# Performance work log

Measured on AMD Instinct MI355X. Metric: run time of the kernel, lower is better.

The kernel has to match this reference:

```python
import jax, jax.numpy as jnp
import numpy as np

DIM = 512


def layer_norm(x, w, b, eps=1e-5):
    mu = jnp.mean(x, axis=-1, keepdims=True)
    var = jnp.var(x, axis=-1, keepdims=True)
    return (x - mu) * jax.lax.rsqrt(var + eps) * w + b


def setup_inputs() -> dict:
    key = jax.random.key(0)
    kx, = jax.random.split(key, 1)
    x = jax.random.normal(kx, (8, 2048, DIM), dtype=jnp.float32)
    ln_w = jnp.ones((DIM,), dtype=jnp.float32)
    ln_b = jnp.zeros((DIM,), dtype=jnp.float32)
    q_diag = jnp.ones((DIM,), dtype=jnp.float32)
    k_diag = jnp.ones((DIM,), dtype=jnp.float32)
    v_diag = jnp.ones((DIM,), dtype=jnp.float32)
    return {"x": x, "ln_w": ln_w, "ln_b": ln_b,
            "q_diag": q_diag, "k_diag": k_diag, "v_diag": v_diag}


def reference(x, ln_w, ln_b, q_diag, k_diag, v_diag):
    # x: [B, N, D]
    xn = layer_norm(x, ln_w, ln_b)
    q = xn * q_diag
    k = xn * k_diag
    v = xn * v_diag
    scale = 1.0 / jnp.sqrt(jnp.float32(xn.shape[-1]))
    sim = jnp.einsum('bnd,bmd->bnm', q, k) * scale  # [B, N, N]
    attn = jax.nn.softmax(sim, axis=-1)
    atn_x = jnp.einsum('bnm,bmd->bnd', attn, v)
    # dropout is identity at inference (p=0)
    return xn + atn_x
```

## Files before the change

kernel.cpp:

```cpp
#include <hip/hip_runtime.h>
#include <hip/hip_bf16.h>
#include <stdint.h>
#include <math.h>

typedef __bf16 bf16_t;
typedef bf16_t bf16x8 __attribute__((ext_vector_type(8)));
typedef float f32x4 __attribute__((ext_vector_type(4)));

#define B_DIM 8
#define N_DIM 2048
#define D_DIM 512
#define QK_SCALE_L2E 0.063758716f
#define M_SHIFT2 5.7707801635558536f

#define KOFF 0
#define VOFF 65536
#define SMEM_ATTN 163840

__device__ __forceinline__ bf16_t f2bf(float f) {
    uint32_t u = __builtin_bit_cast(uint32_t, f);
    u += 0x7FFFu + ((u >> 16) & 1u);
    uint16_t h = (uint16_t)(u >> 16);
    return __builtin_bit_cast(bf16_t, h);
}

__device__ __forceinline__ float fexp2(float x) {
    float r;
    asm("v_exp_f32 %0, %1" : "=v"(r) : "v"(x));
    return r;
}

__global__ __launch_bounds__(512) void prep_fused(
    const float* __restrict__ x, const float* __restrict__ w, const float* __restrict__ bia,
    const float* __restrict__ qd, const float* __restrict__ kd, const float* __restrict__ vd,
    bf16_t* __restrict__ xnb, float* __restrict__ xnf,
    bf16_t* __restrict__ qb, bf16_t* __restrict__ kb, bf16_t* __restrict__ vT)
{
    extern __shared__ char pmem[];
    bf16_t (*vt)[512] = (bf16_t(*)[512])pmem;

    const int bid = blockIdx.x;
    const int b  = bid >> 5;
    const int n0 = (bid & 31) * 64;
    const int tid  = threadIdx.x;
    const int wid  = tid >> 6;
    const int lane = tid & 63;
    const int d    = lane * 8;

    float wv[8], bv[8], qv[8], kv[8], vv[8];
    {
        float4 t;
        t = *(const float4*)(w  + d);     wv[0]=t.x; wv[1]=t.y; wv[2]=t.z; wv[3]=t.w;
        t = *(const float4*)(w  + d + 4); wv[4]=t.x; wv[5]=t.y; wv[6]=t.z; wv[7]=t.w;
        t = *(const float4*)(bia+ d);     bv[0]=t.x; bv[1]=t.y; bv[2]=t.z; bv[3]=t.w;
        t = *(const float4*)(bia+ d + 4); bv[4]=t.x; bv[5]=t.y; bv[6]=t.z; bv[7]=t.w;
        t = *(const float4*)(qd + d);     qv[0]=t.x; qv[1]=t.y; qv[2]=t.z; qv[3]=t.w;
        t = *(const float4*)(qd + d + 4); qv[4]=t.x; qv[5]=t.y; qv[6]=t.z; qv[7]=t.w;
        t = *(const float4*)(kd + d);     kv[0]=t.x; kv[1]=t.y; kv[2]=t.z; kv[3]=t.w;
        t = *(const float4*)(kd + d + 4); kv[4]=t.x; kv[5]=t.y; kv[6]=t.z; kv[7]=t.w;
        t = *(const float4*)(vd + d);     vv[0]=t.x; vv[1]=t.y; vv[2]=t.z; vv[3]=t.w;
        t = *(const float4*)(vd + d + 4); vv[4]=t.x; vv[5]=t.y; vv[6]=t.z; vv[7]=t.w;
    }

    for (int r = 0; r < 8; r++) {
        int nl = wid*8 + r;
        size_t row  = (size_t)b*N_DIM + n0 + nl;
        size_t base = row*D_DIM + d;
        float xv[8];
        {
            float4 a0 = *(const float4*)(x + base);
            float4 a1 = *(const float4*)(x + base + 4);
            xv[0]=a0.x; xv[1]=a0.y; xv[2]=a0.z; xv[3]=a0.w;
            xv[4]=a1.x; xv[5]=a1.y; xv[6]=a1.z; xv[7]=a1.w;
        }
        float s = 0.f, s2 = 0.f;
        #pragma unroll
        for (int j = 0; j < 8; j++) { s += xv[j]; s2 += xv[j]*xv[j]; }
        #pragma unroll
        for (int m = 1; m < 64; m <<= 1) {
            s  += __shfl_xor(s,  m);
            s2 += __shfl_xor(s2, m);
        }
        float mu   = s  * (1.f/512.f);
        float var  = s2 * (1.f/512.f) - mu*mu;
        float rstd = rsqrtf(var + 1e-5f);

        float xo[8];
        bf16x8 qo, ko, xb, vb;
        #pragma unroll
        for (int j = 0; j < 8; j++) {
            float v = (xv[j] - mu) * rstd * wv[j] + bv[j];
            xo[j] = v;
            xb[j] = f2bf(v);
            qo[j] = f2bf(v * qv[j] * QK_SCALE_L2E);
            ko[j] = f2bf(v * kv[j]);
            vb[j] = f2bf(v * vv[j]);
        }
        if (xnb) {
            *(bf16x8*)(xnb + base) = xb;
        } else {
            float4 o0 = {xo[0],xo[1],xo[2],xo[3]};
            float4 o1 = {xo[4],xo[5],xo[6],xo[7]};
            *(float4*)(xnf + base)     = o0;
            *(float4*)(xnf + base + 4) = o1;
        }
        *(bf16x8*)(qb + base) = qo;
        *(bf16x8*)(kb + base) = ko;
        *(bf16x8*)(&vt[nl][d]) = vb;
    }
    __syncthreads();

    {
        const int dd = tid;
        const int salt = (dd >> 1) & 3;
        bf16_t* vrow = vT + ((size_t)(b*D_DIM + dd))*N_DIM + n0;
        #pragma unroll
        for (int kb2 = 0; kb2 < 2; kb2++) {
            #pragma unroll
            for (int sp = 0; sp < 4; sp++) {
                int gg = sp ^ salt;
                bf16x8 o;
                #pragma unroll
                for (int e = 0; e < 4; e++) o[e]   = vt[kb2*32 + 4*gg + e][dd];
                #pragma unroll
                for (int e = 0; e < 4; e++) o[4+e] = vt[kb2*32 + 16 + 4*gg + e][dd];
                *(bf16x8*)(vrow + kb2*32 + sp*8) = o;
            }
        }
    }
}

__global__ __launch_bounds__(512, 2) void attn7(
    const bf16_t* __restrict__ qb, const bf16_t* __restrict__ kb,
    const bf16_t* __restrict__ vT, bf16_t* __restrict__ opart, float* __restrict__ stats)
{
    extern __shared__ char smem[];

    const int bid = blockIdx.x;
    const int xcd = bid & 7, jj = bid >> 3;
    const int grp = xcd + 8*(jj >> 4);
    const int qt  = jj & 15;
    const int b   = grp >> 1;
    const int s   = grp & 1;
    const int q0  = qt * 128;
    const int n0base = s * 1024;

    const int tid  = threadIdx.x;
    const int wid  = tid >> 6;
    const int lane = tid & 63;
    const int g    = lane >> 4;
    const int li   = lane & 15;

    const bf16_t* kb_b = kb + (size_t)b * N_DIM * D_DIM;
    const bf16_t* vT_b = vT + (size_t)b * D_DIM * N_DIM;

    bf16x8 qf[16];
    {
        const bf16_t* qp = qb + ((size_t)(b*N_DIM + q0 + wid*16 + li)) * D_DIM + g*8;
        #pragma unroll
        for (int ks = 0; ks < 16; ks++)
            qf[ks] = *(const bf16x8*)(qp + ks*32);
    }

    f32x4 acc[32];
    const f32x4 zf = {0.f, 0.f, 0.f, 0.f};
    #pragma unroll
    for (int j = 0; j < 32; j++) acc[j] = zf;

    float l_r = 0.f;

    const int Lk = (lane ^ wid) * 8;
    auto stageK = [&](int buf, int t) {
        const int kstart = n0base + t*32;
        char* kdst = smem + KOFF + buf*32768;
        #pragma unroll
        for (int v = 0; v < 4; v++) {
            int row = v*8 + wid;
            const bf16_t* src = kb_b + (size_t)(kstart + row)*D_DIM + Lk;
            __builtin_amdgcn_global_load_lds((const void*)src, (void*)(kdst + row*1024), 16, 0, 0);
        }
    };
    auto stageV = [&](int slot, int t) {
        const int kstart = n0base + t*32;
        char* vdst = smem + VOFF + slot*32768 + wid*4096;
        const int drow = wid*64 + (lane >> 2);
        const bf16_t* src0 = vT_b + (size_t)drow*N_DIM + kstart + (lane & 3)*8;
        #pragma unroll
        for (int v = 0; v < 4; v++) {
            __builtin_amdgcn_global_load_lds((const void*)(src0 + (size_t)(v*16)*N_DIM),
                                             (void*)(vdst + v*1024), 16, 0, 0);
        }
    };

    stageK(0, 0);
    stageV(0, 0);
    asm volatile("s_waitcnt vmcnt(0)" ::: "memory");
    __builtin_amdgcn_s_barrier();

    const int sw  = li & 7;
    const int vsw = (g ^ ((li >> 1) & 3)) << 4;

    int snext = 1, sprev = 2;
    bf16x8 afp = {};

    #pragma unroll 1
    for (int t = 0; t < 32; ++t) {
        const int kbuf = t & 1;

        if (t < 31) {
            stageK(kbuf ^ 1, t + 1);
            stageV(snext, t + 1);
        }
        __builtin_amdgcn_sched_barrier(0);

        const char* kr0 = smem + KOFF + kbuf*32768 + li*1024;
        const char* kr1 = kr0 + 16*1024;
        f32x4 s0 = zf, s1 = zf;
        __builtin_amdgcn_s_setprio(1);
        #pragma unroll
        for (int ks = 0; ks < 16; ks++) {
            int phys = (((ks << 2) + g) ^ sw) << 4;
            bf16x8 k0 = *(const bf16x8*)(kr0 + phys);
            bf16x8 k1 = *(const bf16x8*)(kr1 + phys);
            s0 = __builtin_amdgcn_mfma_f32_16x16x32_bf16(k0, qf[ks], s0, 0, 0, 0);
            s1 = __builtin_amdgcn_mfma_f32_16x16x32_bf16(k1, qf[ks], s1, 0, 0, 0);
        }
        __builtin_amdgcn_s_setprio(0);

        if (t > 0) {
            const char* Vb = smem + VOFF + sprev*32768 + li*64 + vsw;
            __builtin_amdgcn_s_setprio(1);
            #pragma unroll
            for (int j = 0; j < 32; j++) {
                bf16x8 bv = *(const bf16x8*)(Vb + j*1024);
                acc[j] = __builtin_amdgcn_mfma_f32_16x16x32_bf16(afp, bv, acc[j], 0, 0, 0);
            }
            __builtin_amdgcn_s_setprio(0);
        }

        {
            bf16x8 af;
            float la = 0.f, lb2 = 0.f;
            #pragma unroll
            for (int r = 0; r < 4; r++) {
                float e0 = fexp2(s0[r] - M_SHIFT2);
                float e1 = fexp2(s1[r] - M_SHIFT2);
                la += e0; lb2 += e1;
                af[r]   = f2bf(e0);
                af[4+r] = f2bf(e1);
            }
            l_r += la + lb2;
            afp = af;
        }

        sprev = (sprev + 1 == 3) ? 0 : sprev + 1;
        snext = (snext + 1 == 3) ? 0 : snext + 1;

        if (t < 31) {
            asm volatile("s_waitcnt vmcnt(0) lgkmcnt(0)" ::: "memory");
            __builtin_amdgcn_s_barrier();
        }
    }

    {
        const char* Vb = smem + VOFF + sprev*32768 + li*64 + vsw;
        #pragma unroll
        for (int j = 0; j < 32; j++) {
            bf16x8 bv = *(const bf16x8*)(Vb + j*1024);
            acc[j] = __builtin_amdgcn_mfma_f32_16x16x32_bf16(afp, bv, acc[j], 0, 0, 0);
        }
    }

    l_r += __shfl_xor(l_r, 16);
    l_r += __shfl_xor(l_r, 32);

    bf16_t* op = opart + ((size_t)((s*8 + b)*N_DIM) + q0 + wid*16) * D_DIM;
    #pragma unroll
    for (int j = 0; j < 32; j++)
        #pragma unroll
        for (int r = 0; r < 4; r++)
            op[(size_t)(4*g + r)*D_DIM + j*16 + li] = f2bf(acc[j][r]);

    if (lane < 16) {
        stats[(size_t)(s*8 + b)*N_DIM + q0 + wid*16 + lane] = l_r;
    }
}

__global__ __launch_bounds__(256) void merge3(
    const bf16_t* __restrict__ opart, const float* __restrict__ stats,
    const bf16_t* __restrict__ xnb, float* __restrict__ out)
{
    int row  = (int)((blockIdx.x * blockDim.x + threadIdx.x) >> 6);
    int lane = threadIdx.x & 63;
    float l0 = stats[row];
    float l1 = stats[(size_t)16384 + row];
    float rden = 1.f / (l0 + l1);
    size_t base = (size_t)row * D_DIM + lane*8;
    bf16x8 a = *(const bf16x8*)(opart + base);
    bf16x8 c = *(const bf16x8*)(opart + (size_t)16384*D_DIM + base);
    float xv[8];
    if (xnb) {
        bf16x8 xb = *(const bf16x8*)(xnb + base);
        #pragma unroll
        for (int j = 0; j < 8; j++) xv[j] = (float)xb[j];
    } else {
        float4 x0 = *(const float4*)(out + base);
        float4 x1 = *(const float4*)(out + base + 4);
        xv[0]=x0.x; xv[1]=x0.y; xv[2]=x0.z; xv[3]=x0.w;
        xv[4]=x1.x; xv[5]=x1.y; xv[6]=x1.z; xv[7]=x1.w;
    }
    float o[8];
    #pragma unroll
    for (int j = 0; j < 8; j++) o[j] = xv[j] + ((float)a[j] + (float)c[j]) * rden;
    float4 r0 = {o[0], o[1], o[2], o[3]};
    float4 r1 = {o[4], o[5], o[6], o[7]};
    *(float4*)(out + base)     = r0;
    *(float4*)(out + base + 4) = r1;
}

extern "C" void kernel_launch(void* const* d_in, const int* in_sizes, int n_in,
                              void* d_out, int out_size, void* d_ws, size_t ws_size,
                              hipStream_t stream)
{
    const float* x  = (const float*)d_in[0];
    const float* lw = (const float*)d_in[1];
    const float* lb = (const float*)d_in[2];
    const float* qd = (const float*)d_in[3];
    const float* kd = (const float*)d_in[4];
    const float* vd = (const float*)d_in[5];
    float* out = (float*)d_out;

    const size_t MB = 1024u*1024u;
    char* ws = (char*)d_ws;
    bf16_t* qbuf  = (bf16_t*)(ws);
    bf16_t* kbuf  = (bf16_t*)(ws + 16*MB);
    bf16_t* vTb   = (bf16_t*)(ws + 32*MB);
    bf16_t* opart = (bf16_t*)(ws + 48*MB);
    float*  stats = (float*)(ws + 80*MB);
    bf16_t* xnb   = (ws_size >= 97*MB) ? (bf16_t*)(ws + 81*MB) : nullptr;

    hipFuncSetAttribute((const void*)prep_fused, hipFuncAttributeMaxDynamicSharedMemorySize, 65536);
    hipFuncSetAttribute((const void*)attn7, hipFuncAttributeMaxDynamicSharedMemorySize, SMEM_ATTN);

    prep_fused<<<256, 512, 65536, stream>>>(x, lw, lb, qd, kd, vd, xnb, out, qbuf, kbuf, vTb);
    attn7<<<256, 512, SMEM_ATTN, stream>>>(qbuf, kbuf, vTb, opart, stats);
    merge3<<<4096, 256, 0, stream>>>(opart, stats, xnb, out);
}
```

Before: 128.5 us.

## Share softmax probabilities via LDS so each wave computes a D-slice of PV

Each wave now writes its exponentiated score fragment into a double-buffered LDS P tile. For the PV product each wave reads all 128 query rows of P and multiplies them against its own 64-column slice of V, so it holds only four V fragments in registers instead of reading the full V tile. The V staging drops from triple to double buffering, with a partial vmcnt wait before K is prefetched. This cuts per-wave V LDS traffic but adds a P store/load round trip through LDS and changes the output layout. It also changes how loads and barriers overlap.

```diff
diff --git a/kernel.cpp b/kernel.cpp
--- a/kernel.cpp
+++ b/kernel.cpp
@@ -15,7 +15,8 @@
 
 #define KOFF 0
 #define VOFF 65536
-#define SMEM_ATTN 163840
+#define POFF 131072
+#define SMEM_ATTN 147456
 
 __device__ __forceinline__ bf16_t f2bf(float f) {
     uint32_t u = __builtin_bit_cast(uint32_t, f);
@@ -130,7 +131,7 @@
     }
 }
 
-__global__ __launch_bounds__(512, 2) void attn7(
+__global__ __launch_bounds__(512, 2) void attn8(
     const bf16_t* __restrict__ qb, const bf16_t* __restrict__ kb,
     const bf16_t* __restrict__ vT, bf16_t* __restrict__ opart, float* __restrict__ stats)
 {
@@ -180,9 +181,9 @@
             __builtin_amdgcn_global_load_lds((const void*)src, (void*)(kdst + row*1024), 16, 0, 0);
         }
     };
-    auto stageV = [&](int slot, int t) {
+    auto stageV = [&](int buf, int t) {
         const int kstart = n0base + t*32;
-        char* vdst = smem + VOFF + slot*32768 + wid*4096;
+        char* vdst = smem + VOFF + buf*32768 + wid*4096;
         const int drow = wid*64 + (lane >> 2);
         const bf16_t* src0 = vT_b + (size_t)drow*N_DIM + kstart + (lane & 3)*8;
         #pragma unroll
@@ -193,27 +194,26 @@
     };
 
     stageK(0, 0);
-    stageV(0, 0);
     asm volatile("s_waitcnt vmcnt(0)" ::: "memory");
     __builtin_amdgcn_s_barrier();
 
     const int sw  = li & 7;
-    const int vsw = (g ^ ((li >> 1) & 3)) << 4;
-
-    int snext = 1, sprev = 2;
-    bf16x8 afp = {};
+    const int ps  = (li >> 1) & 3;
+    const int psw = (g ^ ps) << 4;
 
     #pragma unroll 1
     for (int t = 0; t < 32; ++t) {
-        const int kbuf = t & 1;
-
-        if (t < 31) {
-            stageK(kbuf ^ 1, t + 1);
-            stageV(snext, t + 1);
-        }
+        const int cb = t & 1;
+        const int pb = cb ^ 1;
+
+        stageV(cb, t);
         __builtin_amdgcn_sched_barrier(0);
-
-        const char* kr0 = smem + KOFF + kbuf*32768 + li*1024;
+        asm volatile("s_waitcnt vmcnt(4)" ::: "memory");
+        __builtin_amdgcn_sched_barrier(0);
+        if (t < 31) stageK(pb, t + 1);
+        __builtin_amdgcn_sched_barrier(0);
+
+        const char* kr0 = smem + KOFF + cb*32768 + li*1024;
         const char* kr1 = kr0 + 16*1024;
         f32x4 s0 = zf, s1 = zf;
         __builtin_amdgcn_s_setprio(1);
@@ -228,59 +228,73 @@
         __builtin_amdgcn_s_setprio(0);
 
         if (t > 0) {
-            const char* Vb = smem + VOFF + sprev*32768 + li*64 + vsw;
+            const char* Pp = smem + POFF + pb*8192;
+            const char* Vp = smem + VOFF + pb*32768 + (size_t)(wid*64 + li)*64 + psw;
+            bf16x8 bv[4];
+            #pragma unroll
+            for (int j = 0; j < 4; j++)
+                bv[j] = *(const bf16x8*)(Vp + j*1024);
             __builtin_amdgcn_s_setprio(1);
             #pragma unroll
-            for (int j = 0; j < 32; j++) {
-                bf16x8 bv = *(const bf16x8*)(Vb + j*1024);
-                acc[j] = __builtin_amdgcn_mfma_f32_16x16x32_bf16(afp, bv, acc[j], 0, 0, 0);
+            for (int m = 0; m < 8; m++) {
+                bf16x8 pa = *(const bf16x8*)(Pp + (m*16 + li)*64 + psw);
+                #pragma unroll
+                for (int j = 0; j < 4; j++)
+                    acc[m*4+j] = __builtin_amdgcn_mfma_f32_16x16x32_bf16(pa, bv[j], acc[m*4+j], 0, 0, 0);
             }
             __builtin_amdgcn_s_setprio(0);
         }
 
         {
-            bf16x8 af;
+            bf16x8 pw;
             float la = 0.f, lb2 = 0.f;
             #pragma unroll
             for (int r = 0; r < 4; r++) {
                 float e0 = fexp2(s0[r] - M_SHIFT2);
                 float e1 = fexp2(s1[r] - M_SHIFT2);
                 la += e0; lb2 += e1;
-                af[r]   = f2bf(e0);
-                af[4+r] = f2bf(e1);
+                pw[r]   = f2bf(e0);
+                pw[4+r] = f2bf(e1);
             }
             l_r += la + lb2;
-            afp = af;
-        }
-
-        sprev = (sprev + 1 == 3) ? 0 : sprev + 1;
-        snext = (snext + 1 == 3) ? 0 : snext + 1;
-
-        if (t < 31) {
-            asm volatile("s_waitcnt vmcnt(0) lgkmcnt(0)" ::: "memory");
-            __builtin_amdgcn_s_barrier();
-        }
-    }
-
+            *(bf16x8*)(smem + POFF + cb*8192 + (size_t)(wid*16 + li)*64 + psw) = pw;
+        }
+
+        asm volatile("s_waitcnt lgkmcnt(0)" ::: "memory");
+        __builtin_amdgcn_s_barrier();
+    }
+
+    asm volatile("s_waitcnt vmcnt(0)" ::: "memory");
     {
-        const char* Vb = smem + VOFF + sprev*32768 + li*64 + vsw;
-        #pragma unroll
-        for (int j = 0; j < 32; j++) {
-            bf16x8 bv = *(const bf16x8*)(Vb + j*1024);
-            acc[j] = __builtin_amdgcn_mfma_f32_16x16x32_bf16(afp, bv, acc[j], 0, 0, 0);
+        const char* Pp = smem + POFF + 1*8192;
+        const char* Vp = smem + VOFF + 1*32768 + (size_t)(wid*64 + li)*64 + psw;
+        bf16x8 bv[4];
+        #pragma unroll
+        for (int j = 0; j < 4; j++)
+            bv[j] = *(const bf16x8*)(Vp + j*1024);
+        #pragma unroll
+        for (int m = 0; m < 8; m++) {
+            bf16x8 pa = *(const bf16x8*)(Pp + (m*16 + li)*64 + psw);
+            #pragma unroll
+            for (int j = 0; j < 4; j++)
+                acc[m*4+j] = __builtin_amdgcn_mfma_f32_16x16x32_bf16(pa, bv[j], acc[m*4+j], 0, 0, 0);
         }
     }
 
     l_r += __shfl_xor(l_r, 16);
     l_r += __shfl_xor(l_r, 32);
 
-    bf16_t* op = opart + ((size_t)((s*8 + b)*N_DIM) + q0 + wid*16) * D_DIM;
+    bf16_t* op = opart + ((size_t)((s*8 + b)*N_DIM) + q0) * D_DIM;
     #pragma unroll
-    for (int j = 0; j < 32; j++)
-        #pragma unroll
-        for (int r = 0; r < 4; r++)
-            op[(size_t)(4*g + r)*D_DIM + j*16 + li] = f2bf(acc[j][r]);
-
+    for (int m = 0; m < 8; m++)
+        #pragma unroll
+        for (int j = 0; j < 4; j++)
+            #pragma unroll
+            for (int r = 0; r < 4; r++) {
+                int qq = m*16 + g*4 + r;
+                int dd = wid*64 + j*16 + li;
+                op[(size_t)qq*D_DIM + dd] = f2bf(acc[m*4+j][r]);
+            }
     if (lane < 16) {
         stats[(size_t)(s*8 + b)*N_DIM + q0 + wid*16 + lane] = l_r;
     }
@@ -340,9 +354,9 @@
     bf16_t* xnb   = (ws_size >= 97*MB) ? (bf16_t*)(ws + 81*MB) : nullptr;
 
     hipFuncSetAttribute((const void*)prep_fused, hipFuncAttributeMaxDynamicSharedMemorySize, 65536);
-    hipFuncSetAttribute((const void*)attn7, hipFuncAttributeMaxDynamicSharedMemorySize, SMEM_ATTN);
+    hipFuncSetAttribute((const void*)attn8, hipFuncAttributeMaxDynamicSharedMemorySize, SMEM_ATTN);
 
     prep_fused<<<256, 512, 65536, stream>>>(x, lw, lb, qd, kd, vd, xnb, out, qbuf, kbuf, vTb);
-    attn7<<<256, 512, SMEM_ATTN, stream>>>(qbuf, kbuf, vTb, opart, stats);
+    attn8<<<256, 512, SMEM_ATTN, stream>>>(qbuf, kbuf, vTb, opart, stats);
     merge3<<<4096, 256, 0, stream>>>(opart, stats, xnb, out);
 }
```

Measured after the change: 139.4 us. 1.08x slower.

## Prefetch K two tiles ahead and drop the one-step-delayed PV software pipeline

Applied to the files above, without the earlier changes.

Restructures the attention loop's buffering. K now uses three smem slots and is prefetched two tiles ahead, while V is double-buffered one tile ahead. The PV MFMA for tile t now runs in the same iteration right after its softmax, replacing the old scheme that deferred PV by one iteration. The waitcnt becomes vmcnt(4) so the outstanding K loads stay in flight across the barrier, giving global loads more latency slack. In exchange, QK and PV of the same tile are serialized within an iteration, so the exp/convert step can stall the matrix pipe.

```diff
diff --git a/kernel.cpp b/kernel.cpp
--- a/kernel.cpp
+++ b/kernel.cpp
@@ -14,7 +14,7 @@
 #define M_SHIFT2 5.7707801635558536f
 
 #define KOFF 0
-#define VOFF 65536
+#define VOFF 98304
 #define SMEM_ATTN 163840
 
 __device__ __forceinline__ bf16_t f2bf(float f) {
@@ -130,7 +130,7 @@
     }
 }
 
-__global__ __launch_bounds__(512, 2) void attn7(
+__global__ __launch_bounds__(512, 2) void attn9(
     const bf16_t* __restrict__ qb, const bf16_t* __restrict__ kb,
     const bf16_t* __restrict__ vT, bf16_t* __restrict__ opart, float* __restrict__ stats)
 {
@@ -170,9 +170,9 @@
     float l_r = 0.f;
 
     const int Lk = (lane ^ wid) * 8;
-    auto stageK = [&](int buf, int t) {
+    auto stageK = [&](int slot, int t) {
         const int kstart = n0base + t*32;
-        char* kdst = smem + KOFF + buf*32768;
+        char* kdst = smem + KOFF + slot*32768;
         #pragma unroll
         for (int v = 0; v < 4; v++) {
             int row = v*8 + wid;
@@ -180,9 +180,9 @@
             __builtin_amdgcn_global_load_lds((const void*)src, (void*)(kdst + row*1024), 16, 0, 0);
         }
     };
-    auto stageV = [&](int slot, int t) {
+    auto stageV = [&](int buf, int t) {
         const int kstart = n0base + t*32;
-        char* vdst = smem + VOFF + slot*32768 + wid*4096;
+        char* vdst = smem + VOFF + buf*32768 + wid*4096;
         const int drow = wid*64 + (lane >> 2);
         const bf16_t* src0 = vT_b + (size_t)drow*N_DIM + kstart + (lane & 3)*8;
         #pragma unroll
@@ -194,26 +194,25 @@
 
     stageK(0, 0);
     stageV(0, 0);
-    asm volatile("s_waitcnt vmcnt(0)" ::: "memory");
+    stageK(1, 1);
+    asm volatile("s_waitcnt vmcnt(4)" ::: "memory");
     __builtin_amdgcn_s_barrier();
 
     const int sw  = li & 7;
     const int vsw = (g ^ ((li >> 1) & 3)) << 4;
 
-    int snext = 1, sprev = 2;
-    bf16x8 afp = {};
+    int kc = 0;
 
     #pragma unroll 1
     for (int t = 0; t < 32; ++t) {
-        const int kbuf = t & 1;
-
-        if (t < 31) {
-            stageK(kbuf ^ 1, t + 1);
-            stageV(snext, t + 1);
-        }
+        const int vbuf = t & 1;
+        const int ks2  = (kc + 2 >= 3) ? (kc + 2 - 3) : (kc + 2);
+
+        if (t < 31) stageV(vbuf ^ 1, t + 1);
+        if (t < 30) stageK(ks2, t + 2);
         __builtin_amdgcn_sched_barrier(0);
 
-        const char* kr0 = smem + KOFF + kbuf*32768 + li*1024;
+        const char* kr0 = smem + KOFF + kc*32768 + li*1024;
         const char* kr1 = kr0 + 16*1024;
         f32x4 s0 = zf, s1 = zf;
         __builtin_amdgcn_s_setprio(1);
@@ -227,48 +226,36 @@
         }
         __builtin_amdgcn_s_setprio(0);
 
-        if (t > 0) {
-            const char* Vb = smem + VOFF + sprev*32768 + li*64 + vsw;
-            __builtin_amdgcn_s_setprio(1);
-            #pragma unroll
-            for (int j = 0; j < 32; j++) {
-                bf16x8 bv = *(const bf16x8*)(Vb + j*1024);
-                acc[j] = __builtin_amdgcn_mfma_f32_16x16x32_bf16(afp, bv, acc[j], 0, 0, 0);
-            }
-            __builtin_amdgcn_s_setprio(0);
-        }
-
-        {
-            bf16x8 af;
-            float la = 0.f, lb2 = 0.f;
-            #pragma unroll
-            for (int r = 0; r < 4; r++) {
-                float e0 = fexp2(s0[r] - M_SHIFT2);
-                float e1 = fexp2(s1[r] - M_SHIFT2);
-                la += e0; lb2 += e1;
-                af[r]   = f2bf(e0);
-                af[4+r] = f2bf(e1);
-            }
-            l_r += la + lb2;
-            afp = af;
-        }
-
-        sprev = (sprev + 1 == 3) ? 0 : sprev + 1;
-        snext = (snext + 1 == 3) ? 0 : snext + 1;
-
-        if (t < 31) {
-            asm volatile("s_waitcnt vmcnt(0) lgkmcnt(0)" ::: "memory");
-            __builtin_amdgcn_s_barrier();
-        }
-    }
-
-    {
-        const char* Vb = smem + VOFF + sprev*32768 + li*64 + vsw;
+        float p0[4], p1[4];
+        #pragma unroll
+        for (int r = 0; r < 4; r++) {
+            p0[r] = fexp2(s0[r] - M_SHIFT2);
+            p1[r] = fexp2(s1[r] - M_SHIFT2);
+        }
+        l_r += ((p0[0]+p0[1]) + (p0[2]+p0[3])) + ((p1[0]+p1[1]) + (p1[2]+p1[3]));
+        bf16x8 af;
+        af[0]=f2bf(p0[0]); af[1]=f2bf(p0[1]); af[2]=f2bf(p0[2]); af[3]=f2bf(p0[3]);
+        af[4]=f2bf(p1[0]); af[5]=f2bf(p1[1]); af[6]=f2bf(p1[2]); af[7]=f2bf(p1[3]);
+
+        const char* Vb = smem + VOFF + vbuf*32768 + li*64 + vsw;
+        __builtin_amdgcn_s_setprio(1);
         #pragma unroll
         for (int j = 0; j < 32; j++) {
             bf16x8 bv = *(const bf16x8*)(Vb + j*1024);
-            acc[j] = __builtin_amdgcn_mfma_f32_16x16x32_bf16(afp, bv, acc[j], 0, 0, 0);
-        }
+            acc[j] = __builtin_amdgcn_mfma_f32_16x16x32_bf16(af, bv, acc[j], 0, 0, 0);
+        }
+        __builtin_amdgcn_s_setprio(0);
+
+        if (t < 31) {
+            if (t < 30) {
+                asm volatile("s_waitcnt vmcnt(4) lgkmcnt(0)" ::: "memory");
+            } else {
+                asm volatile("s_waitcnt vmcnt(0) lgkmcnt(0)" ::: "memory");
+            }
+            __builtin_amdgcn_s_barrier();
+        }
+
+        kc = (kc + 1 >= 3) ? 0 : kc + 1;
     }
 
     l_r += __shfl_xor(l_r, 16);
@@ -340,9 +327,9 @@
     bf16_t* xnb   = (ws_size >= 97*MB) ? (bf16_t*)(ws + 81*MB) : nullptr;
 
     hipFuncSetAttribute((const void*)prep_fused, hipFuncAttributeMaxDynamicSharedMemorySize, 65536);
-    hipFuncSetAttribute((const void*)attn7, hipFuncAttributeMaxDynamicSharedMemorySize, SMEM_ATTN);
+    hipFuncSetAttribute((const void*)attn9, hipFuncAttributeMaxDynamicSharedMemorySize, SMEM_ATTN);
 
     prep_fused<<<256, 512, 65536, stream>>>(x, lw, lb, qd, kd, vd, xnb, out, qbuf, kbuf, vTb);
-    attn7<<<256, 512, SMEM_ATTN, stream>>>(qbuf, kbuf, vTb, opart, stats);
+    attn9<<<256, 512, SMEM_ATTN, stream>>>(qbuf, kbuf, vTb, opart, stats);
     merge3<<<4096, 256, 0, stream>>>(opart, stats, xnb, out);
 }
```

After: 122.9 us (median of 2 runs). 1.05x faster.
